# Kernel tuning notes

Hardware: AMD Instinct MI355X
Metric: run time of the kernel (lower is better)

## Reference

```python
import jax, jax.numpy as jnp
import numpy as np

B, C, Z, E = 2, 32, 4, 2
N = C * C * Z  # 4096 grid points per element
P_TH, T_TH = 0.5, 0.5
ELE_D = (0.74, 0.528)


def _consts():
    real_size = jnp.array([25.0, 25.0, 3.0], jnp.float32)
    lattice = real_size / jnp.array([C, C, Z], jnp.float32)
    g = jnp.stack(jnp.meshgrid(jnp.arange(C), jnp.arange(C), jnp.arange(Z), indexing='ij'), axis=-1)
    pit = g.reshape(N, 3).astype(jnp.float32)
    return pit, lattice


def _cdist(a, b):
    # a [M,3], b [K,3] -> [M,K] euclidean distance
    d2 = jnp.sum((a[:, None, :] - b[None, :, :]) ** 2, axis=-1)
    return jnp.sqrt(d2)


def _nms(pos, conf, valid, ele_d):
    # Fixed-shape version of Analyzer.nms: sort by confidence desc (invalid -> -inf, sorts last),
    # triu(<d) adjacency restricted to valid points, matrix-multiply suppression correction.
    key = jnp.where(valid, conf, -jnp.inf)
    order = jnp.argsort(-key)              # descending confidence
    pos_s = pos[order]
    valid_s = valid[order]
    dist = _cdist(pos_s, pos_s)            # [N,N] ~ 64 MB
    iu = jnp.triu(jnp.ones((N, N), bool), k=1)
    adj = ((dist < ele_d) & iu & valid_s[:, None] & valid_s[None, :]).astype(pos.dtype)
    restrain = adj.sum(0)                  # col sums: # earlier neighbors
    restrain_one = (restrain != 0).astype(pos.dtype)
    correct = restrain_one @ adj           # earlier neighbors that are themselves suppressed
    sel = ((restrain - correct) == 0) & valid_s
    keep = jnp.zeros(N, bool).at[order].set(sel)
    return keep & valid


def _match(t_pos, t_valid, p_pos, p_valid, ele_d):
    # TP matching: T point is matched if any valid P within ele_d; argmin gives its P partner.
    dist = _cdist(t_pos, p_pos)            # [N,N]
    dist = jnp.where(t_valid[:, None] & p_valid[None, :], dist, jnp.inf)
    tp_t_mask = (dist < ele_d).any(1)      # rows in torch's TP_T_index
    tp_p_idx = jnp.argmin(dist, axis=1).astype(jnp.int32)  # torch's TP_P_index (valid where tp_t_mask)
    return tp_t_mask, tp_p_idx


def setup_inputs() -> dict:
    key = jax.random.key(0)
    k1, k2 = jax.random.split(key)
    predictions = jax.random.uniform(k1, (B, C, C, Z, E, 4), jnp.float32)
    targets = jax.random.uniform(k2, (B, C, C, Z, E, 4), jnp.float32)
    return {"predictions": predictions, "targets": targets}


def reference(predictions, targets):
    pit, lattice = _consts()
    # [B,C,C,Z,E,4] -> [B,E,N,4]
    pred = predictions.reshape(B, C, C, Z, E, 4).transpose(0, 4, 1, 2, 3, 5).reshape(B, E, N, 4)
    tgt = targets.reshape(B, C, C, Z, E, 4).transpose(0, 4, 1, 2, 3, 5).reshape(B, E, N, 4)

    p_pos = (pred[..., :3] + pit) * lattice    # [B,E,N,3] absolute coords
    p_conf = pred[..., 3]
    mask_p = p_conf > P_TH
    t_pos = (tgt[..., :3] + pit) * lattice
    mask_t = tgt[..., 3] > T_TH

    keeps, tpt, tpp, tptn, tppn = [], [], [], [], []
    for e in range(E):
        d = ELE_D[e]
        keep_e = jax.vmap(lambda p, c, v: _nms(p, c, v, d))(p_pos[:, e], p_conf[:, e], mask_p[:, e])
        tt, tp = jax.vmap(lambda tq, tv, pq, pv: _match(tq, tv, pq, pv, d))(
            t_pos[:, e], mask_t[:, e], p_pos[:, e], mask_p[:, e])
        ttn, tpn = jax.vmap(lambda tq, tv, pq, pv: _match(tq, tv, pq, pv, d))(
            t_pos[:, e], mask_t[:, e], p_pos[:, e], keep_e)
        keeps.append(keep_e); tpt.append(tt); tpp.append(tp); tptn.append(ttn); tppn.append(tpn)

    keep_nms = jnp.stack(keeps, 1)   # [B,E,N] combined mask_p & nms keep
    tp_t_mask = jnp.stack(tpt, 1)
    tp_p_idx = jnp.stack(tpp, 1)
    tp_t_mask_nms = jnp.stack(tptn, 1)
    tp_p_idx_nms = jnp.stack(tppn, 1)

    return (p_pos, mask_p, keep_nms, t_pos, mask_t,
            tp_t_mask, tp_p_idx, tp_t_mask_nms, tp_p_idx_nms)
```

## Files before the change

kernel.cpp:

```cpp
#include <hip/hip_runtime.h>
#include <cmath>
#include <cstdint>

namespace {
constexpr int NPT  = 4096;

constexpr int O_PPOS  = 0;
constexpr int O_MASKP = 49152;
constexpr int O_KEEP  = 65536;
constexpr int O_TPOS  = 81920;
constexpr int O_MASKT = 131072;
constexpr int O_TPT   = 147456;
constexpr int O_TPP   = 163840;
constexpr int O_TPTN  = 180224;
constexpr int O_TPPN  = 196608;

constexpr float GUARD = 1.4999f;
}

__device__ __forceinline__ unsigned long long shfl_xor_u64(unsigned long long v, int m) {
    unsigned lo = (unsigned)v, hi = (unsigned)(v >> 32);
    lo = __shfl_xor(lo, m); hi = __shfl_xor(hi, m);
    return ((unsigned long long)hi << 32) | lo;
}

__device__ __forceinline__ float3 cellpos(float4 p, int n) {
#pragma clang fp contract(off)
    float fx = (float)(n >> 7), fy = (float)((n >> 2) & 31), fz = (float)(n & 3);
    float3 r;
    r.x = (p.x + fx) * 0.78125f;
    r.y = (p.y + fy) * 0.78125f;
    r.z = (p.z + fz) * 0.75f;
    return r;
}
__device__ __forceinline__ float dist2(float3 a, float3 b) {
#pragma clang fp contract(off)
    float dx = a.x - b.x, dy = a.y - b.y, dz = a.z - b.z;
    float d2 = dx * dx + dy * dy;
    return d2 + dz * dz;
}

__device__ __forceinline__ unsigned restrain_of(const float4* __restrict__ pred,
                                                int base4, int pn, float se) {
#pragma clang fp contract(off)
    float4 p = pred[base4 + pn * 2];
    if (!(p.w > 0.5f)) return 0u;
    float3 pj = cellpos(p, pn);
    int gx = pn >> 7, gy = (pn >> 2) & 31;
    unsigned c = 0;
    for (int q = 0; q < 9; ++q) {
        int nx = gx + q / 3 - 1, ny = gy + q % 3 - 1;
        if ((unsigned)nx > 31u || (unsigned)ny > 31u) continue;
        int nb = nx * 128 + ny * 4;
#pragma unroll
        for (int nz = 0; nz < 4; ++nz) {
            int ni = nb + nz;
            float4 pi = pred[base4 + ni * 2];
            float3 qi = cellpos(pi, ni);
            float d2 = dist2(pj, qi);
            bool prec = (pi.w > p.w) || ((pi.w == p.w) && (ni < pn));
            if ((pi.w > 0.5f) && (d2 < se) && prec) c++;
        }
    }
    return c;
}

__device__ __noinline__ bool keep_of(const float4* __restrict__ pred,
                                     int base4, int k, float se) {
#pragma clang fp contract(off)
    float4 p = pred[base4 + k * 2];
    if (!(p.w > 0.5f)) return false;
    float3 pj = cellpos(p, k);
    int gx = k >> 7, gy = (k >> 2) & 31;
    for (int q = 0; q < 9; ++q) {
        int nx = gx + q / 3 - 1, ny = gy + q % 3 - 1;
        if ((unsigned)nx > 31u || (unsigned)ny > 31u) continue;
        int nb = nx * 128 + ny * 4;
        for (int nz = 0; nz < 4; ++nz) {
            int ni = nb + nz;
            float4 pi = pred[base4 + ni * 2];
            float3 qi = cellpos(pi, ni);
            float d2 = dist2(pj, qi);
            bool prec = (pi.w > p.w) || ((pi.w == p.w) && (ni < k));
            if ((pi.w > 0.5f) && (d2 < se) && prec &&
                restrain_of(pred, base4, ni, se) == 0u)
                return false;
        }
    }
    return true;
}

__global__ void __launch_bounds__(512) k_all(const float4* __restrict__ pred,
                                             const float4* __restrict__ tgt,
                                             float* __restrict__ out,
                                             float s0, float s1) {
#pragma clang fp contract(off)
    __shared__ float4 pp[9 * 24 * 4];
    __shared__ unsigned char restr[7 * 22 * 4];
    __shared__ unsigned char keepl[5 * 20 * 4];
    int bid = blockIdx.x;
    int h2 = bid & 1, gx = (bid >> 1) & 31, s = bid >> 6;
    int b = s >> 1, e = s & 1;
    int base4 = b * 8192 + e;
    float se = (s & 1) ? s1 : s0;
    int gy0 = h2 << 4;
    int t = (int)threadIdx.x;

    for (int i = t; i < 864; i += 512) {
        int rx = i / 96, rem = i - rx * 96, ry = rem >> 2, z = rem & 3;
        int px = gx + rx - 4, py = gy0 + ry - 4;
        float4 v = {0.0f, 0.0f, 0.0f, -1.0f};
        if ((unsigned)px < 32u && (unsigned)py < 32u) {
            int pn = px * 128 + py * 4 + z;
            float4 p = pred[base4 + pn * 2];
            float3 c = cellpos(p, pn);
            v.x = c.x; v.y = c.y; v.z = c.z; v.w = p.w;
        }
        pp[i] = v;
    }
    __syncthreads();

    for (int ra = t; ra < 616; ra += 512) {
        int ax = ra / 88, rem = ra - ax * 88, ay = rem >> 2, z = rem & 3;
        int px = gx + ax - 3, py = gy0 + ay - 3;
        float4 p = pp[((ax + 1) * 24 + (ay + 1)) * 4 + z];
        unsigned c = 0;
        if (p.w > 0.5f) {
            int pn = px * 128 + py * 4 + z;
            float3 pj = {p.x, p.y, p.z};
            for (int q = 0; q < 9; ++q) {
                int dx = q / 3 - 1, dy = q % 3 - 1;
                int nb = (px + dx) * 128 + (py + dy) * 4;
                const float4* pc = &pp[((ax + 1 + dx) * 24 + (ay + 1 + dy)) * 4];
#pragma unroll
                for (int nz = 0; nz < 4; ++nz) {
                    float4 pi = pc[nz];
                    int ni = nb + nz;
                    float3 qi = {pi.x, pi.y, pi.z};
                    float d2 = dist2(pj, qi);
                    bool prec = (pi.w > p.w) || ((pi.w == p.w) && (ni < pn));
                    if ((pi.w > 0.5f) && (d2 < se) && prec) c++;
                }
            }
        }
        restr[ra] = (unsigned char)c;
    }
    __syncthreads();

    for (int kb = t; kb < 400; kb += 512) {
        int kx = kb / 80, rem = kb - kx * 80, ky = rem >> 2, z = rem & 3;
        int px = gx + kx - 2, py = gy0 + ky - 2;
        float4 p = pp[((kx + 2) * 24 + (ky + 2)) * 4 + z];
        bool valid = p.w > 0.5f;
        int pn = px * 128 + py * 4 + z;
        unsigned any = 0;
        if (valid) {
            float3 pj = {p.x, p.y, p.z};
            for (int q = 0; q < 9; ++q) {
                int dx = q / 3 - 1, dy = q % 3 - 1;
                int nb = (px + dx) * 128 + (py + dy) * 4;
                const float4* pc = &pp[((kx + 2 + dx) * 24 + (ky + 2 + dy)) * 4];
                const unsigned char* lr =
                    &restr[((kx + 1 + dx) * 22 + (ky + 1 + dy)) * 4];
#pragma unroll
                for (int nz = 0; nz < 4; ++nz) {
                    float4 pi = pc[nz];
                    int ni = nb + nz;
                    float3 qi = {pi.x, pi.y, pi.z};
                    float d2 = dist2(pj, qi);
                    bool prec = (pi.w > p.w) || ((pi.w == p.w) && (ni < pn));
                    if ((pi.w > 0.5f) && (lr[nz] == 0) && (d2 < se) && prec) any = 1u;
                }
            }
        }
        bool keep = valid && (any == 0);
        keepl[kb] = keep ? 1 : 0;
        if (kx == 2 && ky >= 2 && ky < 18) {
            int row = s * NPT + pn;
            out[O_PPOS + row * 3 + 0] = p.x;
            out[O_PPOS + row * 3 + 1] = p.y;
            out[O_PPOS + row * 3 + 2] = p.z;
            out[O_MASKP + row] = valid ? 1.0f : 0.0f;
            out[O_KEEP + row]  = keep ? 1.0f : 0.0f;
        }
    }
    __syncthreads();

    int r = t >> 3, h = t & 7;
    int gyy = r >> 2, z = r & 3;
    int gy = gy0 + gyy;
    int n = (gx << 7) + (gy << 2) + z;
    int row = s * NPT + n;
    float4 t4 = tgt[base4 + n * 2];
    float3 tj = cellpos(t4, n);
    bool tv = t4.w > 0.5f;
    if (h == 0) {
        out[O_TPOS + row * 3 + 0] = tj.x;
        out[O_TPOS + row * 3 + 1] = tj.y;
        out[O_TPOS + row * 3 + 2] = tj.z;
        out[O_MASKT + row] = tv ? 1.0f : 0.0f;
    }
    if (!tv) {
        if (h == 0) {
            out[O_TPT + row] = 0.0f; out[O_TPTN + row] = 0.0f;
            out[O_TPP + row] = 0.0f; out[O_TPPN + row] = 0.0f;
        }
        return;
    }
    unsigned long long bs = ~0ull, bn = ~0ull;
    unsigned as_ = 0, an_ = 0;
    for (int qq = 0; qq < 4; ++qq) {
        int q = qq * 8 + h;
        if (q > 24) continue;
        int dx = q / 5 - 2, dy = q % 5 - 2;
        int nb = (gx + dx) * 128 + (gy + dy) * 4;
        const float4* pc = &pp[((dx + 4) * 24 + (gyy + dy + 4)) * 4];
        const unsigned char* lk = &keepl[((dx + 2) * 20 + (gyy + dy + 2)) * 4];
#pragma unroll
        for (int nz = 0; nz < 4; ++nz) {
            float4 pi = pc[nz];
            int ni = nb + nz;
            float3 qi = {pi.x, pi.y, pi.z};
            float d2 = dist2(tj, qi);
            float dist = sqrtf(d2);
            unsigned long long enc =
                ((unsigned long long)__float_as_uint(dist) << 32) | (unsigned)ni;
            if (pi.w > 0.5f) { if (enc < bs) bs = enc; if (d2 < se) as_ = 1u; }
            if (lk[nz]) { if (enc < bn) bn = enc; if (d2 < se) an_ = 1u; }
        }
    }
    for (int m = 1; m < 8; m <<= 1) {
        unsigned long long o = shfl_xor_u64(bs, m); if (o < bs) bs = o;
        o = shfl_xor_u64(bn, m); if (o < bn) bn = o;
        as_ |= __shfl_xor(as_, m);
        an_ |= __shfl_xor(an_, m);
    }
    bool acc_s = __uint_as_float((unsigned)(bs >> 32)) < GUARD;
    bool acc_n = __uint_as_float((unsigned)(bn >> 32)) < GUARD;
    if (!(acc_s && acc_n)) {
        unsigned long long fs = ~0ull, fn = ~0ull;
        for (int k = h; k < NPT; k += 8) {
            float4 pi = pred[base4 + k * 2];
            float3 qi = cellpos(pi, k);
            float d2 = dist2(tj, qi);
            float dist = sqrtf(d2);
            unsigned long long enc =
                ((unsigned long long)__float_as_uint(dist) << 32) | (unsigned)k;
            if (pi.w > 0.5f && enc < fs) fs = enc;
            if (enc < fn && keep_of(pred, base4, k, se)) fn = enc;
        }
        for (int m = 1; m < 8; m <<= 1) {
            unsigned long long o = shfl_xor_u64(fs, m); if (o < fs) fs = o;
            o = shfl_xor_u64(fn, m); if (o < fn) fn = o;
        }
        bs = fs; bn = fn;
    }
    if (h == 0) {
        out[O_TPT + row]  = as_ ? 1.0f : 0.0f;
        out[O_TPTN + row] = an_ ? 1.0f : 0.0f;
        out[O_TPP + row]  = (float)((bs == ~0ull) ? 0u : (unsigned)(bs & 0xffffffffull));
        out[O_TPPN + row] = (float)((bn == ~0ull) ? 0u : (unsigned)(bn & 0xffffffffull));
    }
}

static float sq_boundary(float t) {
    float f = (float)((double)t * (double)t);
    while (sqrtf(f) >= t) f = nextafterf(f, 0.0f);
    while (sqrtf(f) < t)  f = nextafterf(f, __builtin_inff());
    return f;
}

extern "C" void kernel_launch(void* const* d_in, const int* in_sizes, int n_in,
                              void* d_out, int out_size, void* d_ws, size_t ws_size,
                              hipStream_t stream) {
    (void)in_sizes; (void)n_in; (void)out_size; (void)d_ws; (void)ws_size;
    const float4* pred = (const float4*)d_in[0];
    const float4* tgt  = (const float4*)d_in[1];
    float* out = (float*)d_out;

    float s0 = sq_boundary(0.74f);
    float s1 = sq_boundary(0.528f);

    k_all<<<dim3(256), dim3(512), 0, stream>>>(pred, tgt, out, s0, s1);
}
```

Baseline: 70.00 us.

## Split blocks into 8-row y tiles, prune z neighbors, and prefetch targets early

Each block now covers an 8-row y strip instead of 16, which doubles the grid to 512 blocks and shrinks the shared halo tiles. The NMS restrain and keep passes only check z neighbours within ±1, fully unroll their 3x3 loops, and run in a single pass guarded by thread count. The match phase uses 16 lanes per target point, and each target load is issued before the first barrier so its latency overlaps the shared-memory fill. The trade-off is more halo recomputation relative to useful work, and the z pruning is only correct if the distance thresholds rule out points two z cells apart.

```diff
diff --git a/kernel.cpp b/kernel.cpp
--- a/kernel.cpp
+++ b/kernel.cpp
@@ -90,24 +90,28 @@
     return true;
 }
 
-__global__ void __launch_bounds__(512) k_all(const float4* __restrict__ pred,
-                                             const float4* __restrict__ tgt,
-                                             float* __restrict__ out,
-                                             float s0, float s1) {
-#pragma clang fp contract(off)
-    __shared__ float4 pp[9 * 24 * 4];
-    __shared__ unsigned char restr[7 * 22 * 4];
-    __shared__ unsigned char keepl[5 * 20 * 4];
+__global__ void __launch_bounds__(512, 4) k_all(const float4* __restrict__ pred,
+                                                const float4* __restrict__ tgt,
+                                                float* __restrict__ out,
+                                                float s0, float s1) {
+#pragma clang fp contract(off)
+    __shared__ float4 pp[9 * 16 * 4];
+    __shared__ unsigned char restr[7 * 14 * 4];
+    __shared__ unsigned char keepl[5 * 12 * 4];
     int bid = blockIdx.x;
-    int h2 = bid & 1, gx = (bid >> 1) & 31, s = bid >> 6;
+    int gy0 = (bid & 3) << 3, gx = (bid >> 2) & 31, s = bid >> 7;
     int b = s >> 1, e = s & 1;
     int base4 = b * 8192 + e;
     float se = (s & 1) ? s1 : s0;
-    int gy0 = h2 << 4;
     int t = (int)threadIdx.x;
 
-    for (int i = t; i < 864; i += 512) {
-        int rx = i / 96, rem = i - rx * 96, ry = rem >> 2, z = rem & 3;
+    int rr = t >> 4, hh = t & 15;
+    int gyy_c = rr >> 2, z_c = rr & 3;
+    int n_c = (gx << 7) + ((gy0 + gyy_c) << 2) + z_c;
+    float4 t4 = tgt[base4 + n_c * 2];
+
+    for (int i = t; i < 576; i += 512) {
+        int rx = i >> 6, rem = i & 63, ry = rem >> 2, z = rem & 3;
         int px = gx + rx - 4, py = gy0 + ry - 4;
         float4 v = {0.0f, 0.0f, 0.0f, -1.0f};
         if ((unsigned)px < 32u && (unsigned)py < 32u) {
@@ -120,62 +124,71 @@
     }
     __syncthreads();
 
-    for (int ra = t; ra < 616; ra += 512) {
-        int ax = ra / 88, rem = ra - ax * 88, ay = rem >> 2, z = rem & 3;
+    if (t < 392) {
+        int ax = t / 56, rem = t - ax * 56, ay = rem >> 2, z = rem & 3;
         int px = gx + ax - 3, py = gy0 + ay - 3;
-        float4 p = pp[((ax + 1) * 24 + (ay + 1)) * 4 + z];
+        float4 p = pp[((ax + 1) * 16 + (ay + 1)) * 4 + z];
         unsigned c = 0;
         if (p.w > 0.5f) {
             int pn = px * 128 + py * 4 + z;
             float3 pj = {p.x, p.y, p.z};
+#pragma unroll
             for (int q = 0; q < 9; ++q) {
                 int dx = q / 3 - 1, dy = q % 3 - 1;
                 int nb = (px + dx) * 128 + (py + dy) * 4;
-                const float4* pc = &pp[((ax + 1 + dx) * 24 + (ay + 1 + dy)) * 4];
-#pragma unroll
-                for (int nz = 0; nz < 4; ++nz) {
-                    float4 pi = pc[nz];
+                const float4* pc = &pp[((ax + 1 + dx) * 16 + (ay + 1 + dy)) * 4];
+#pragma unroll
+                for (int dz = -1; dz <= 1; ++dz) {
+                    int nz = z + dz;
+                    int nzc = nz < 0 ? 0 : (nz > 3 ? 3 : nz);
+                    float4 pi = pc[nzc];
                     int ni = nb + nz;
                     float3 qi = {pi.x, pi.y, pi.z};
                     float d2 = dist2(pj, qi);
+                    bool zok = (unsigned)nz < 4u;
                     bool prec = (pi.w > p.w) || ((pi.w == p.w) && (ni < pn));
-                    if ((pi.w > 0.5f) && (d2 < se) && prec) c++;
+                    if (zok && (pi.w > 0.5f) && (d2 < se) && prec) c++;
                 }
             }
         }
-        restr[ra] = (unsigned char)c;
+        restr[t] = (unsigned char)c;
     }
     __syncthreads();
 
-    for (int kb = t; kb < 400; kb += 512) {
-        int kx = kb / 80, rem = kb - kx * 80, ky = rem >> 2, z = rem & 3;
+    if (t < 240) {
+        int kx = t / 48, rem = t - kx * 48, ky = rem >> 2, z = rem & 3;
         int px = gx + kx - 2, py = gy0 + ky - 2;
-        float4 p = pp[((kx + 2) * 24 + (ky + 2)) * 4 + z];
+        float4 p = pp[((kx + 2) * 16 + (ky + 2)) * 4 + z];
         bool valid = p.w > 0.5f;
         int pn = px * 128 + py * 4 + z;
         unsigned any = 0;
         if (valid) {
             float3 pj = {p.x, p.y, p.z};
+#pragma unroll
             for (int q = 0; q < 9; ++q) {
                 int dx = q / 3 - 1, dy = q % 3 - 1;
                 int nb = (px + dx) * 128 + (py + dy) * 4;
-                const float4* pc = &pp[((kx + 2 + dx) * 24 + (ky + 2 + dy)) * 4];
+                const float4* pc = &pp[((kx + 2 + dx) * 16 + (ky + 2 + dy)) * 4];
                 const unsigned char* lr =
-                    &restr[((kx + 1 + dx) * 22 + (ky + 1 + dy)) * 4];
-#pragma unroll
-                for (int nz = 0; nz < 4; ++nz) {
-                    float4 pi = pc[nz];
+                    &restr[((kx + 1 + dx) * 14 + (ky + 1 + dy)) * 4];
+#pragma unroll
+                for (int dz = -1; dz <= 1; ++dz) {
+                    int nz = z + dz;
+                    int nzc = nz < 0 ? 0 : (nz > 3 ? 3 : nz);
+                    float4 pi = pc[nzc];
                     int ni = nb + nz;
                     float3 qi = {pi.x, pi.y, pi.z};
                     float d2 = dist2(pj, qi);
+                    bool zok = (unsigned)nz < 4u;
                     bool prec = (pi.w > p.w) || ((pi.w == p.w) && (ni < pn));
-                    if ((pi.w > 0.5f) && (lr[nz] == 0) && (d2 < se) && prec) any = 1u;
+                    if (zok && (pi.w > 0.5f) && (lr[nzc] == 0) && (d2 < se) && prec)
+                        any = 1u;
                 }
             }
         }
         bool keep = valid && (any == 0);
-        keepl[kb] = keep ? 1 : 0;
-        if (kx == 2 && ky >= 2 && ky < 18) {
+        keepl[t] = keep ? 1 : 0;
+        if (kx == 2 && ky >= 2 && ky < 10) {
             int row = s * NPT + pn;
             out[O_PPOS + row * 3 + 0] = p.x;
             out[O_PPOS + row * 3 + 1] = p.y;
@@ -186,12 +199,10 @@
     }
     __syncthreads();
 
-    int r = t >> 3, h = t & 7;
-    int gyy = r >> 2, z = r & 3;
+    int gyy = gyy_c, z = z_c, h = hh;
     int gy = gy0 + gyy;
-    int n = (gx << 7) + (gy << 2) + z;
+    int n = n_c;
     int row = s * NPT + n;
-    float4 t4 = tgt[base4 + n * 2];
     float3 tj = cellpos(t4, n);
     bool tv = t4.w > 0.5f;
     if (h == 0) {
@@ -209,13 +220,14 @@
     }
     unsigned long long bs = ~0ull, bn = ~0ull;
     unsigned as_ = 0, an_ = 0;
-    for (int qq = 0; qq < 4; ++qq) {
-        int q = qq * 8 + h;
+#pragma unroll
+    for (int pass = 0; pass < 2; ++pass) {
+        int q = pass * 16 + h;
         if (q > 24) continue;
         int dx = q / 5 - 2, dy = q % 5 - 2;
         int nb = (gx + dx) * 128 + (gy + dy) * 4;
-        const float4* pc = &pp[((dx + 4) * 24 + (gyy + dy + 4)) * 4];
-        const unsigned char* lk = &keepl[((dx + 2) * 20 + (gyy + dy + 2)) * 4];
+        const float4* pc = &pp[((dx + 4) * 16 + (gyy + dy + 4)) * 4];
+        const unsigned char* lk = &keepl[((dx + 2) * 12 + (gyy + dy + 2)) * 4];
 #pragma unroll
         for (int nz = 0; nz < 4; ++nz) {
             float4 pi = pc[nz];
@@ -229,7 +241,7 @@
             if (lk[nz]) { if (enc < bn) bn = enc; if (d2 < se) an_ = 1u; }
         }
     }
-    for (int m = 1; m < 8; m <<= 1) {
+    for (int m = 1; m < 16; m <<= 1) {
         unsigned long long o = shfl_xor_u64(bs, m); if (o < bs) bs = o;
         o = shfl_xor_u64(bn, m); if (o < bn) bn = o;
         as_ |= __shfl_xor(as_, m);
@@ -239,7 +251,7 @@
     bool acc_n = __uint_as_float((unsigned)(bn >> 32)) < GUARD;
     if (!(acc_s && acc_n)) {
         unsigned long long fs = ~0ull, fn = ~0ull;
-        for (int k = h; k < NPT; k += 8) {
+        for (int k = h; k < NPT; k += 16) {
             float4 pi = pred[base4 + k * 2];
             float3 qi = cellpos(pi, k);
             float d2 = dist2(tj, qi);
@@ -249,7 +261,7 @@
             if (pi.w > 0.5f && enc < fs) fs = enc;
             if (enc < fn && keep_of(pred, base4, k, se)) fn = enc;
         }
-        for (int m = 1; m < 8; m <<= 1) {
+        for (int m = 1; m < 16; m <<= 1) {
             unsigned long long o = shfl_xor_u64(fs, m); if (o < fs) fs = o;
             o = shfl_xor_u64(fn, m); if (o < fn) fn = o;
         }
@@ -281,5 +293,5 @@
     float s0 = sq_boundary(0.74f);
     float s1 = sq_boundary(0.528f);
 
-    k_all<<<dim3(256), dim3(512), 0, stream>>>(pred, tgt, out, s0, s1);
-}
+    k_all<<<dim3(512), dim3(512), 0, stream>>>(pred, tgt, out, s0, s1);
+}
```

Measured after the change: 64.85 us. -7.4%, faster.
